# Kernel tuning notes

Measured on AMD Instinct MI355X. Metric: run time of the kernel, lower is better.

The kernel has to match this reference:

```python
import jax, jax.numpy as jnp
import numpy as np

E = 400000          # total child edges in the ready batch
P = 100000          # number of parent nodes (segments)
D = 256             # 2 * model_dim


def setup_inputs() -> dict:
    key = jax.random.key(0)
    ks = jax.random.split(key, 6)
    child_hs = jax.random.normal(ks[0], (E, D), dtype=jnp.float32)
    child_cs = jax.random.normal(ks[1], (E, D), dtype=jnp.float32)
    segment_ids = jnp.sort(jax.random.randint(ks[2], (E,), 0, P))
    W_gates = jax.random.normal(ks[3], (D, 3 * D), dtype=jnp.float32) * (1.0 / np.sqrt(D))
    b_gates = jnp.zeros((3 * D,), dtype=jnp.float32)
    W_f = jax.random.normal(ks[4], (D, D), dtype=jnp.float32) * (1.0 / np.sqrt(D))
    b_f = jnp.zeros((D,), dtype=jnp.float32)
    return {
        "child_hs": child_hs,
        "child_cs": child_cs,
        "segment_ids": segment_ids,
        "num_segments": P,
        "W_gates": W_gates,
        "b_gates": b_gates,
        "W_f": W_f,
        "b_f": b_f,
    }


def reference(child_hs, child_cs, segment_ids, num_segments, W_gates, b_gates, W_f, b_f):
    # child_hs_sum per parent (segment reduce over children)
    hs_sum = jax.ops.segment_sum(child_hs, segment_ids, num_segments=num_segments)  # [P, D]
    # gates = Linear(2*model_dim -> 6*model_dim), chunk into i, o, g
    gates = hs_sum @ W_gates + b_gates                         # [P, 3D]
    i, o, g = jnp.split(gates, 3, axis=1)
    i, o, g = jax.nn.sigmoid(i), jax.nn.sigmoid(o), jnp.tanh(g)
    # per-child forget gates, fc = f * c, segment-reduced per parent
    f = jax.nn.sigmoid(child_hs @ W_f + b_f)                   # [E, D]
    fc = jax.ops.segment_sum(f * child_cs, segment_ids, num_segments=num_segments)  # [P, D]
    # child-sum LSTM update
    c = i * g + fc
    h = o * jnp.tanh(c)
    return h, c
```

## Files before the change

### kernel.cpp

```cpp
#include <hip/hip_runtime.h>
#include <hip/hip_bf16.h>

typedef __attribute__((ext_vector_type(8))) short short8;
typedef __attribute__((ext_vector_type(4))) float floatx4;

#define DD 256

__device__ __forceinline__ unsigned short f2bf(float f) {
    unsigned int u = __builtin_bit_cast(unsigned int, f);
    u += 0x7FFFu + ((u >> 16) & 1u);
    return (unsigned short)(u >> 16);
}

__device__ __forceinline__ float sigm(float x) { return 1.0f / (1.0f + __expf(-x)); }
__device__ __forceinline__ float tanh_fast(float x) { return 2.0f / (1.0f + __expf(-2.0f * x)) - 1.0f; }

__global__ void pack_weights(const float* __restrict__ W_f, const float* __restrict__ W_g,
                             unsigned short* __restrict__ WfT, unsigned short* __restrict__ WgT) {
    int idx = blockIdx.x * 256 + threadIdx.x;
    if (idx < 65536) {
        int n = idx >> 8, k = idx & 255;
        WfT[idx] = f2bf(W_f[k * 256 + n]);
    } else {
        int i2 = idx - 65536;
        int n = i2 >> 8, k = i2 & 255;
        WgT[i2] = f2bf(W_g[k * 768 + n]);
    }
}

__global__ void build_start(const int* __restrict__ seg, int E, int P, int* __restrict__ start) {
    int e = blockIdx.x * blockDim.x + threadIdx.x;
    if (e >= E) return;
    int s = seg[e];
    if (e == 0) {
        for (int p = 0; p <= s; ++p) start[p] = 0;
    } else {
        int sp = seg[e - 1];
        for (int p = sp + 1; p <= s; ++p) start[p] = e;
    }
    if (e == E - 1) {
        for (int p = s + 1; p <= P; ++p) start[p] = E;
    }
}

__global__ void hs_reduce(const float* __restrict__ child_hs, const int* __restrict__ start,
                          int P, float* __restrict__ hs_sum) {
    int wave = threadIdx.x >> 6, lane = threadIdx.x & 63;
    int p = blockIdx.x * 4 + wave;
    if (p >= P) return;
    int lo = start[p], hi = start[p + 1];
    float4 acc = make_float4(0.f, 0.f, 0.f, 0.f);
    const float4* src = (const float4*)child_hs;
    for (int e = lo; e < hi; ++e) {
        float4 v = src[(size_t)e * 64 + lane];
        acc.x += v.x; acc.y += v.y; acc.z += v.z; acc.w += v.w;
    }
    ((float4*)hs_sum)[(size_t)p * 64 + lane] = acc;
}

__global__ __launch_bounds__(256, 2) void gemm1_fc(
    const float* __restrict__ child_hs, const float* __restrict__ child_cs,
    const int* __restrict__ seg, const unsigned short* __restrict__ WfT,
    const float* __restrict__ b_f, float* __restrict__ fc, int E) {
    __shared__ __align__(16) unsigned short ldsB[8192];
    const int tid = threadIdx.x;
    const int w = tid >> 6, lane = tid & 63;
    const int nl = lane & 15, q = lane >> 4;
    const int e_base = blockIdx.x * 64 + w * 16;

    floatx4 acc[16];
#pragma unroll
    for (int t = 0; t < 16; ++t) acc[t] = (floatx4){0.f, 0.f, 0.f, 0.f};

    const float* Arow = child_hs + (size_t)(e_base + nl) * DD;

    for (int ks = 0; ks < 8; ++ks) {
#pragma unroll
        for (int r = 0; r < 4; ++r) {
            int chunk = tid + r * 256;
            int n = chunk >> 2, qb = chunk & 3;
            uint4 v = *(const uint4*)(WfT + n * 256 + ks * 32 + qb * 8);
            int dst = ((n >> 4) << 6) + (qb << 4) + (n & 15);
            ((uint4*)ldsB)[dst] = v;
        }
        float4 a0 = *(const float4*)(Arow + ks * 32 + q * 8);
        float4 a1 = *(const float4*)(Arow + ks * 32 + q * 8 + 4);
        short8 af;
        af[0] = (short)f2bf(a0.x); af[1] = (short)f2bf(a0.y);
        af[2] = (short)f2bf(a0.z); af[3] = (short)f2bf(a0.w);
        af[4] = (short)f2bf(a1.x); af[5] = (short)f2bf(a1.y);
        af[6] = (short)f2bf(a1.z); af[7] = (short)f2bf(a1.w);
        __syncthreads();
#pragma unroll
        for (int t = 0; t < 16; ++t) {
            short8 bf = ((const short8*)ldsB)[t * 64 + lane];
            acc[t] = __builtin_amdgcn_mfma_f32_16x16x32_bf16(af, bf, acc[t], 0, 0, 0);
        }
        __syncthreads();
    }

    int e0 = e_base + q * 4;
    int s0 = seg[e0], s1 = seg[e0 + 1], s2 = seg[e0 + 2], s3 = seg[e0 + 3];
#pragma unroll
    for (int t = 0; t < 16; ++t) {
        int n = t * 16 + nl;
        float bias = b_f[n];
        float v0 = sigm(acc[t][0] + bias) * child_cs[(size_t)(e0 + 0) * DD + n];
        float v1 = sigm(acc[t][1] + bias) * child_cs[(size_t)(e0 + 1) * DD + n];
        float v2 = sigm(acc[t][2] + bias) * child_cs[(size_t)(e0 + 2) * DD + n];
        float v3 = sigm(acc[t][3] + bias) * child_cs[(size_t)(e0 + 3) * DD + n];
        float a = v0; int s = s0;
        if (s1 == s) { a += v1; } else { atomicAdd(&fc[(size_t)s * DD + n], a); a = v1; s = s1; }
        if (s2 == s) { a += v2; } else { atomicAdd(&fc[(size_t)s * DD + n], a); a = v2; s = s2; }
        if (s3 == s) { a += v3; } else { atomicAdd(&fc[(size_t)s * DD + n], a); a = v3; s = s3; }
        atomicAdd(&fc[(size_t)s * DD + n], a);
    }
}

__global__ __launch_bounds__(256, 2) void gemm2_lstm(
    const float* __restrict__ hs_sum, const unsigned short* __restrict__ WgT,
    const float* __restrict__ b_g, float* __restrict__ h_out, float* __restrict__ c_out, int P) {
    const int tid = threadIdx.x;
    const int w = tid >> 6, lane = tid & 63;
    const int nl = lane & 15, q = lane >> 4;
    const int p_base = blockIdx.x * 16;
    const int cg0 = w * 4;

    floatx4 acc[12];
#pragma unroll
    for (int t = 0; t < 12; ++t) acc[t] = (floatx4){0.f, 0.f, 0.f, 0.f};

    const float* Arow = hs_sum + (size_t)(p_base + nl) * DD;

    for (int ks = 0; ks < 8; ++ks) {
        float4 a0 = *(const float4*)(Arow + ks * 32 + q * 8);
        float4 a1 = *(const float4*)(Arow + ks * 32 + q * 8 + 4);
        short8 af;
        af[0] = (short)f2bf(a0.x); af[1] = (short)f2bf(a0.y);
        af[2] = (short)f2bf(a0.z); af[3] = (short)f2bf(a0.w);
        af[4] = (short)f2bf(a1.x); af[5] = (short)f2bf(a1.y);
        af[6] = (short)f2bf(a1.z); af[7] = (short)f2bf(a1.w);
#pragma unroll
        for (int cgl = 0; cgl < 4; ++cgl) {
            int cg = cg0 + cgl;
#pragma unroll
            for (int part = 0; part < 3; ++part) {
                int nrow = part * 256 + cg * 16 + nl;
                short8 bf = *(const short8*)(WgT + nrow * 256 + ks * 32 + q * 8);
                acc[cgl * 3 + part] =
                    __builtin_amdgcn_mfma_f32_16x16x32_bf16(af, bf, acc[cgl * 3 + part], 0, 0, 0);
            }
        }
    }

    __syncthreads();

#pragma unroll
    for (int cgl = 0; cgl < 4; ++cgl) {
        int n = (cg0 + cgl) * 16 + nl;
        float bi = b_g[n], bo = b_g[256 + n], bg = b_g[512 + n];
#pragma unroll
        for (int reg = 0; reg < 4; ++reg) {
            int p = p_base + q * 4 + reg;
            float I = acc[cgl * 3 + 0][reg] + bi;
            float O = acc[cgl * 3 + 1][reg] + bo;
            float G = acc[cgl * 3 + 2][reg] + bg;
            float iv = sigm(I), ov = sigm(O), gv = tanh_fast(G);
            float c = iv * gv + c_out[(size_t)p * DD + n];
            float hv = ov * tanh_fast(c);
            h_out[(size_t)p * DD + n] = hv;
            c_out[(size_t)p * DD + n] = c;
        }
    }
}

extern "C" void kernel_launch(void* const* d_in, const int* in_sizes, int n_in,
                              void* d_out, int out_size, void* d_ws, size_t ws_size,
                              hipStream_t stream) {
    const float* child_hs = (const float*)d_in[0];
    const float* child_cs = (const float*)d_in[1];
    const int*   seg      = (const int*)d_in[2];
    const float* W_gates  = (const float*)d_in[4];
    const float* b_gates  = (const float*)d_in[5];
    const float* W_f      = (const float*)d_in[6];
    const float* b_f      = (const float*)d_in[7];

    const int D = 256;
    const int E = in_sizes[0] / D;
    const int P = out_size / (2 * D);

    float* h_out = (float*)d_out;
    float* c_out = (float*)d_out + (size_t)P * D;

    unsigned short* WfT = (unsigned short*)d_ws;
    unsigned short* WgT = WfT + 65536;
    int* start = (int*)(WgT + 196608);

    hipMemsetAsync(c_out, 0, (size_t)P * D * sizeof(float), stream);

    pack_weights<<<1024, 256, 0, stream>>>(W_f, W_gates, WfT, WgT);
    build_start<<<(E + 255) / 256, 256, 0, stream>>>(seg, E, P, start);
    hs_reduce<<<(P + 3) / 4, 256, 0, stream>>>(child_hs, start, P, h_out);
    gemm1_fc<<<E / 64, 256, 0, stream>>>(child_hs, child_cs, seg, WfT, b_f, c_out, E);
    gemm2_lstm<<<P / 16, 256, 0, stream>>>(h_out, WgT, b_gates, h_out, c_out, P);
}
```

Measured before the change: 1.488 ms.

## Stage gate weights in LDS and enlarge gemm2 tile to 64 rows

```diff
diff --git a/kernel.cpp b/kernel.cpp
--- a/kernel.cpp
+++ b/kernel.cpp
@@ -117,59 +117,83 @@
     }
 }
 
-__global__ __launch_bounds__(256, 2) void gemm2_lstm(
+__global__ __launch_bounds__(512, 2) void gemm2_lstm(
     const float* __restrict__ hs_sum, const unsigned short* __restrict__ WgT,
     const float* __restrict__ b_g, float* __restrict__ h_out, float* __restrict__ c_out, int P) {
+    __shared__ __align__(16) unsigned short ldsB[24576];
     const int tid = threadIdx.x;
     const int w = tid >> 6, lane = tid & 63;
+    const int wr = w >> 2, wc = w & 3;
     const int nl = lane & 15, q = lane >> 4;
-    const int p_base = blockIdx.x * 16;
-    const int cg0 = w * 4;
-
-    floatx4 acc[12];
-#pragma unroll
-    for (int t = 0; t < 12; ++t) acc[t] = (floatx4){0.f, 0.f, 0.f, 0.f};
-
-    const float* Arow = hs_sum + (size_t)(p_base + nl) * DD;
+    const int p_base = blockIdx.x * 64;
+
+    floatx4 acc[2][12];
+#pragma unroll
+    for (int rt = 0; rt < 2; ++rt)
+#pragma unroll
+        for (int t = 0; t < 12; ++t) acc[rt][t] = (floatx4){0.f, 0.f, 0.f, 0.f};
+
+    const float* Arow0 = hs_sum + (size_t)(p_base + wr * 32 + nl) * DD;
+    const float* Arow1 = Arow0 + (size_t)16 * DD;
 
     for (int ks = 0; ks < 8; ++ks) {
-        float4 a0 = *(const float4*)(Arow + ks * 32 + q * 8);
-        float4 a1 = *(const float4*)(Arow + ks * 32 + q * 8 + 4);
-        short8 af;
-        af[0] = (short)f2bf(a0.x); af[1] = (short)f2bf(a0.y);
-        af[2] = (short)f2bf(a0.z); af[3] = (short)f2bf(a0.w);
-        af[4] = (short)f2bf(a1.x); af[5] = (short)f2bf(a1.y);
-        af[6] = (short)f2bf(a1.z); af[7] = (short)f2bf(a1.w);
+#pragma unroll
+        for (int r = 0; r < 6; ++r) {
+            int chunk = tid + r * 512;
+            int n = chunk >> 2, qb = chunk & 3;
+            uint4 v = *(const uint4*)(WgT + n * 256 + ks * 32 + qb * 8);
+            int dst = ((n >> 4) << 6) + (qb << 4) + (n & 15);
+            ((uint4*)ldsB)[dst] = v;
+        }
+        float4 a0 = *(const float4*)(Arow0 + ks * 32 + q * 8);
+        float4 a1 = *(const float4*)(Arow0 + ks * 32 + q * 8 + 4);
+        float4 a2 = *(const float4*)(Arow1 + ks * 32 + q * 8);
+        float4 a3 = *(const float4*)(Arow1 + ks * 32 + q * 8 + 4);
+        short8 af0, af1;
+        af0[0] = (short)f2bf(a0.x); af0[1] = (short)f2bf(a0.y);
+        af0[2] = (short)f2bf(a0.z); af0[3] = (short)f2bf(a0.w);
+        af0[4] = (short)f2bf(a1.x); af0[5] = (short)f2bf(a1.y);
+        af0[6] = (short)f2bf(a1.z); af0[7] = (short)f2bf(a1.w);
+        af1[0] = (short)f2bf(a2.x); af1[1] = (short)f2bf(a2.y);
+        af1[2] = (short)f2bf(a2.z); af1[3] = (short)f2bf(a2.w);
+        af1[4] = (short)f2bf(a3.x); af1[5] = (short)f2bf(a3.y);
+        af1[6] = (short)f2bf(a3.z); af1[7] = (short)f2bf(a3.w);
+        __syncthreads();
 #pragma unroll
         for (int cgl = 0; cgl < 4; ++cgl) {
-            int cg = cg0 + cgl;
 #pragma unroll
             for (int part = 0; part < 3; ++part) {
-                int nrow = part * 256 + cg * 16 + nl;
-                short8 bf = *(const short8*)(WgT + nrow * 256 + ks * 32 + q * 8);
-                acc[cgl * 3 + part] =
-                    __builtin_amdgcn_mfma_f32_16x16x32_bf16(af, bf, acc[cgl * 3 + part], 0, 0, 0);
+                int t = part * 16 + (wc * 4 + cgl);
+                short8 bf = ((const short8*)ldsB)[t * 64 + lane];
+                acc[0][cgl * 3 + part] =
+                    __builtin_amdgcn_mfma_f32_16x16x32_bf16(af0, bf, acc[0][cgl * 3 + part], 0, 0, 0);
+                acc[1][cgl * 3 + part] =
+                    __builtin_amdgcn_mfma_f32_16x16x32_bf16(af1, bf, acc[1][cgl * 3 + part], 0, 0, 0);
             }
         }
-    }
-
-    __syncthreads();
-
-#pragma unroll
-    for (int cgl = 0; cgl < 4; ++cgl) {
-        int n = (cg0 + cgl) * 16 + nl;
-        float bi = b_g[n], bo = b_g[256 + n], bg = b_g[512 + n];
-#pragma unroll
-        for (int reg = 0; reg < 4; ++reg) {
-            int p = p_base + q * 4 + reg;
-            float I = acc[cgl * 3 + 0][reg] + bi;
-            float O = acc[cgl * 3 + 1][reg] + bo;
-            float G = acc[cgl * 3 + 2][reg] + bg;
-            float iv = sigm(I), ov = sigm(O), gv = tanh_fast(G);
-            float c = iv * gv + c_out[(size_t)p * DD + n];
-            float hv = ov * tanh_fast(c);
-            h_out[(size_t)p * DD + n] = hv;
-            c_out[(size_t)p * DD + n] = c;
+        __syncthreads();
+    }
+
+#pragma unroll
+    for (int rt = 0; rt < 2; ++rt) {
+#pragma unroll
+        for (int cgl = 0; cgl < 4; ++cgl) {
+            int n = (wc * 4 + cgl) * 16 + nl;
+            float bi = b_g[n], bo = b_g[256 + n], bg = b_g[512 + n];
+#pragma unroll
+            for (int reg = 0; reg < 4; ++reg) {
+                int p = p_base + wr * 32 + rt * 16 + q * 4 + reg;
+                if (p < P) {
+                    float I = acc[rt][cgl * 3 + 0][reg] + bi;
+                    float O = acc[rt][cgl * 3 + 1][reg] + bo;
+                    float G = acc[rt][cgl * 3 + 2][reg] + bg;
+                    float iv = sigm(I), ov = sigm(O), gv = tanh_fast(G);
+                    float c = iv * gv + c_out[(size_t)p * DD + n];
+                    float hv = ov * tanh_fast(c);
+                    h_out[(size_t)p * DD + n] = hv;
+                    c_out[(size_t)p * DD + n] = c;
+                }
+            }
         }
     }
 }
@@ -202,5 +226,5 @@
     build_start<<<(E + 255) / 256, 256, 0, stream>>>(seg, E, P, start);
     hs_reduce<<<(P + 3) / 4, 256, 0, stream>>>(child_hs, start, P, h_out);
     gemm1_fc<<<E / 64, 256, 0, stream>>>(child_hs, child_cs, seg, WfT, b_f, c_out, E);
-    gemm2_lstm<<<P / 16, 256, 0, stream>>>(h_out, WgT, b_gates, h_out, c_out, P);
-}
+    gemm2_lstm<<<(P + 63) / 64, 512, 0, stream>>>(h_out, WgT, b_gates, h_out, c_out, P);
+}
```

After: 1.402 ms. -5.8%, faster.
